# Kernel optimization log

Measured on AMD Instinct MI355X. Metric: run time of the kernel, lower is better.

## Reference

```python
import jax, jax.numpy as jnp
import numpy as np

D_MODEL = 1024
H = 16
D_K = D_MODEL // H  # 64


def setup_inputs() -> dict:
    key = jax.random.key(0)
    ks = jax.random.split(key, 10)
    s = 1.0 / np.sqrt(D_MODEL)
    x = jax.random.normal(ks[0], (4, 2048, D_MODEL), dtype=jnp.float32)
    # Per-head linear weights stacked: [H, d_model, d_k]
    Wq = jax.random.uniform(ks[1], (H, D_MODEL, D_K), jnp.float32, -s, s)
    bq = jax.random.uniform(ks[2], (H, D_K), jnp.float32, -s, s)
    Wk = jax.random.uniform(ks[3], (H, D_MODEL, D_K), jnp.float32, -s, s)
    bk = jax.random.uniform(ks[4], (H, D_K), jnp.float32, -s, s)
    Wv = jax.random.uniform(ks[5], (H, D_MODEL, D_K), jnp.float32, -s, s)
    bv = jax.random.uniform(ks[6], (H, D_K), jnp.float32, -s, s)
    so = 1.0 / np.sqrt(H * D_K)
    Wo = jax.random.uniform(ks[7], (H * D_K, D_MODEL), jnp.float32, -so, so)
    bo = jax.random.uniform(ks[8], (D_MODEL,), jnp.float32, -so, so)
    return {"x": x, "Wq": Wq, "bq": bq, "Wk": Wk, "bk": bk, "Wv": Wv, "bv": bv, "Wo": Wo, "bo": bo}


def reference(x, Wq, bq, Wk, bk, Wv, bv, Wo, bo):
    # x: [B, S, D]; Wq/Wk/Wv: [H, D, d_k]; b*: [H, d_k]
    q = jnp.einsum('bsd,hdk->bhsk', x, Wq) + bq[None, :, None, :]
    k = jnp.einsum('bsd,hdk->bhsk', x, Wk) + bk[None, :, None, :]
    v = jnp.einsum('bsd,hdk->bhsk', x, Wv) + bv[None, :, None, :]
    scores = jnp.einsum('bhqk,bhsk->bhqs', q, k) / np.sqrt(D_K)
    S = x.shape[1]
    causal = jnp.triu(jnp.ones((S, S), dtype=bool), k=1)  # True above diagonal
    scores = jnp.where(causal, -jnp.inf, scores)
    attn = jax.nn.softmax(scores, axis=-1)
    ctx = jnp.einsum('bhqs,bhsk->bhqk', attn, v)  # [B, H, S, d_k]
    B = x.shape[0]
    # concat heads: torch cats head outputs along last dim -> [B, S, H*d_k]
    ctx = jnp.transpose(ctx, (0, 2, 1, 3)).reshape(B, S, H * D_K)
    return ctx @ Wo + bo
```

## Files before the change

kernel.cpp:

```cpp
#include <hip/hip_runtime.h>
#include <hip/hip_bf16.h>

typedef unsigned short u16;
typedef __attribute__((ext_vector_type(8))) short short8;
typedef __attribute__((ext_vector_type(4))) short short4v;
typedef __attribute__((ext_vector_type(4))) float floatx4;

#define D_MODEL 1024
#define NH 16
#define SEQ 2048
#define BATCH 4
#define M_ROWS 8192
#define N_QKV 3072
#define PS_LD 72

__device__ __forceinline__ u16 f2u(float f) {
    __hip_bfloat16 h = __float2bfloat16(f);
    u16 u; __builtin_memcpy(&u, &h, 2); return u;
}

__device__ __forceinline__ void async_copy16(const u16* g, u16* l) {
    __builtin_amdgcn_global_load_lds(
        (const __attribute__((address_space(1))) unsigned int*)(g),
        (__attribute__((address_space(3))) unsigned int*)(l),
        16, 0, 0);
}

__global__ __launch_bounds__(256) void prep(
    const float* __restrict__ x,
    const float* __restrict__ Wq, const float* __restrict__ Wk,
    const float* __restrict__ Wv, const float* __restrict__ Wo,
    const float* __restrict__ bq, const float* __restrict__ bk,
    const float* __restrict__ bv, const float* __restrict__ bo,
    u16* __restrict__ xb, u16* __restrict__ Wpt, u16* __restrict__ Wot,
    float* __restrict__ biasp)
{
    __shared__ u16 T[64 * 72];
    const int tid = threadIdx.x;
    const int blk = blockIdx.x;

    if (blk < 4096) {
        size_t i = ((size_t)blk * 256 + tid) * 8;
        float4 f0 = *(const float4*)&x[i];
        float4 f1 = *(const float4*)&x[i + 4];
        u16 t[8] = {f2u(f0.x), f2u(f0.y), f2u(f0.z), f2u(f0.w),
                    f2u(f1.x), f2u(f1.y), f2u(f1.z), f2u(f1.w)};
        *(short8*)&xb[i] = *(short8*)t;
        return;
    }
    if (blk == 5120) {
        #pragma unroll
        for (int j = 0; j < 16; j++) {
            int idx = j * 256 + tid;
            float v;
            if (idx < 1024)      v = bq[idx] * 0.125f;
            else if (idx < 2048) v = bk[idx - 1024];
            else if (idx < 3072) v = bv[idx - 2048];
            else                 v = bo[idx - 3072];
            biasp[idx] = v;
        }
        return;
    }
    const int wb = blk - 4096;
    const int r = tid >> 2, s4 = (tid & 3) * 16;
    if (wb < 768) {
        int sel = wb / 256, rem = wb % 256;
        int h = rem >> 4, ktile = rem & 15;
        const float* W = (sel == 0) ? Wq : ((sel == 1) ? Wk : Wv);
        const float scale = (sel == 0) ? 0.125f : 1.0f;
        const float* src = W + ((size_t)h * 1024 + ktile * 64 + r) * 64 + s4;
        #pragma unroll
        for (int i = 0; i < 16; i++) T[(s4 + i) * 72 + r] = f2u(src[i] * scale);
        __syncthreads();
        u16 tmp[16];
        #pragma unroll
        for (int i = 0; i < 16; i++) tmp[i] = T[r * 72 + s4 + i];
        u16* dst = Wpt + ((size_t)sel * 1024 + h * 64 + r) * 1024 + ktile * 64 + s4;
        *(short8*)&dst[0] = *(short8*)&tmp[0];
        *(short8*)&dst[8] = *(short8*)&tmp[8];
    } else {
        int rem = wb - 768;
        int nt = rem >> 4, kt2 = rem & 15;
        const float* src = Wo + ((size_t)kt2 * 64 + r) * 1024 + nt * 64 + s4;
        #pragma unroll
        for (int i = 0; i < 16; i++) T[(s4 + i) * 72 + r] = f2u(src[i]);
        __syncthreads();
        u16 tmp[16];
        #pragma unroll
        for (int i = 0; i < 16; i++) tmp[i] = T[r * 72 + s4 + i];
        u16* dst = Wot + ((size_t)nt * 64 + r) * 1024 + kt2 * 64 + s4;
        *(short8*)&dst[0] = *(short8*)&tmp[0];
        *(short8*)&dst[8] = *(short8*)&tmp[8];
    }
}

__global__ __launch_bounds__(256) void vtrans(const u16* __restrict__ QKV,
                                              u16* __restrict__ Vtg) {
    __shared__ u16 T[64 * 72];
    const int bh = blockIdx.x, kt = blockIdx.y;
    const int b = bh >> 4, h = bh & 15;
    const int tid = threadIdx.x;
    const int r = tid >> 2, s4 = (tid & 3) * 16;
    const u16* vp = QKV + (size_t)(b * SEQ + kt * 64 + r) * N_QKV + 2 * D_MODEL + h * 64 + s4;
    *(short8*)&T[r * 72 + s4]     = *(const short8*)&vp[0];
    *(short8*)&T[r * 72 + s4 + 8] = *(const short8*)&vp[8];
    __syncthreads();
    u16 tmp[16];
    #pragma unroll
    for (int i = 0; i < 16; i++) tmp[i] = T[(s4 + i) * 72 + r];
    u16* op = Vtg + ((size_t)bh * 64 + r) * SEQ + kt * 64 + s4;
    *(short8*)&op[0] = *(short8*)&tmp[0];
    *(short8*)&op[8] = *(short8*)&tmp[8];
}

template <typename OT>
__global__ __launch_bounds__(256) void gemm128(
    const u16* __restrict__ A, const u16* __restrict__ Bt,
    const float* __restrict__ bias, OT* __restrict__ C,
    int M, int N, int K)
{
    __shared__ u16 As[128 * 64];
    __shared__ u16 Bs[128 * 64];
    const int tid = threadIdx.x;
    const int w = tid >> 6, lane = tid & 63;
    const int l16 = lane & 15, quad = lane >> 4;
    const int bn = blockIdx.x * 128, bm = blockIdx.y * 128;
    const int wr = (w >> 1) * 64, wc = (w & 1) * 64;

    floatx4 acc[4][4];
    #pragma unroll
    for (int i = 0; i < 4; i++)
        #pragma unroll
        for (int j = 0; j < 4; j++) acc[i][j] = (floatx4){0.f, 0.f, 0.f, 0.f};

    for (int k0 = 0; k0 < K; k0 += 64) {
        #pragma unroll
        for (int c = 0; c < 4; c++) {
            const int off = (w * 4 + c) * 1024 + lane * 16;
            const int row = off >> 7, seg = (off >> 4) & 7;
            async_copy16(A  + (size_t)(bm + row) * K + k0 + seg * 8, &As[(w * 4 + c) * 512]);
            async_copy16(Bt + (size_t)(bn + row) * K + k0 + seg * 8, &Bs[(w * 4 + c) * 512]);
        }
        __syncthreads();
        #pragma unroll
        for (int kc = 0; kc < 2; kc++) {
            short8 a[4], b[4];
            #pragma unroll
            for (int i = 0; i < 4; i++)
                a[i] = *(short8*)&As[(wr + i * 16 + l16) * 64 + kc * 32 + quad * 8];
            #pragma unroll
            for (int i = 0; i < 4; i++)
                b[i] = *(short8*)&Bs[(wc + i * 16 + l16) * 64 + kc * 32 + quad * 8];
            #pragma unroll
            for (int mm = 0; mm < 4; mm++)
                #pragma unroll
                for (int nn = 0; nn < 4; nn++)
                    acc[mm][nn] = __builtin_amdgcn_mfma_f32_16x16x32_bf16(
                        a[mm], b[nn], acc[mm][nn], 0, 0, 0);
        }
        __syncthreads();
    }

    #pragma unroll
    for (int nn = 0; nn < 4; nn++) {
        const int col = bn + wc + nn * 16 + l16;
        const float bi = bias[col];
        #pragma unroll
        for (int mm = 0; mm < 4; mm++) {
            const int row = bm + wr + mm * 16 + quad * 4;
            #pragma unroll
            for (int r = 0; r < 4; r++) {
                float v = acc[mm][nn][r] + bi;
                if constexpr (sizeof(OT) == 2) ((u16*)C)[(size_t)(row + r) * N + col] = f2u(v);
                else                           C[(size_t)(row + r) * N + col] = v;
            }
        }
    }
}

__global__ __launch_bounds__(256) void attn_mfma(
    const u16* __restrict__ QKV, const u16* __restrict__ Vtg, u16* __restrict__ ctx)
{
    __shared__ u16 Ks[2][64 * 64];
    __shared__ u16 Vs[2][64 * 64];
    __shared__ u16 Ps[128 * PS_LD];

    const int bh = blockIdx.x;
    const int qt = (int)(gridDim.y - 1) - (int)blockIdx.y;
    const int b = bh >> 4, h = bh & 15;
    const int tid = threadIdx.x;
    const int w = tid >> 6, lane = tid & 63;
    const int l16 = lane & 15, quad = lane >> 4;

    const int r0 = tid >> 3,        c0 = tid & 7;
    const int r1 = (256 + tid) >> 3, c1 = tid & 7;
    const int sw0 = c0 ^ (r0 & 7), sw1 = c1 ^ (r1 & 7);

    short8 q[2][2];
    #pragma unroll
    for (int m = 0; m < 2; m++) {
        const u16* qp = QKV + (size_t)(b * SEQ + qt * 128 + w * 32 + m * 16 + l16) * N_QKV + h * 64;
        q[m][0] = *(const short8*)&qp[quad * 8];
        q[m][1] = *(const short8*)&qp[32 + quad * 8];
    }

    floatx4 O[2][4];
    #pragma unroll
    for (int m = 0; m < 2; m++)
        #pragma unroll
        for (int i = 0; i < 4; i++) O[m][i] = (floatx4){0.f, 0.f, 0.f, 0.f};
    float li[2] = {0.f, 0.f};

    const int nkt = 2 * qt + 2;
    const int qrow_w_max = qt * 128 + w * 32 + 31;

    const size_t kbase = (size_t)(b * SEQ) * N_QKV + D_MODEL + h * 64;
    const size_t vbase = (size_t)bh * 64 * SEQ;

    {
        float4 ka = *(const float4*)(QKV + kbase + (size_t)(0 + r0) * N_QKV + c0 * 8);
        float4 kb = *(const float4*)(QKV + kbase + (size_t)(0 + r1) * N_QKV + c1 * 8);
        float4 va = *(const float4*)(Vtg + vbase + (size_t)r0 * SEQ + 0 + c0 * 8);
        float4 vb = *(const float4*)(Vtg + vbase + (size_t)r1 * SEQ + 0 + c1 * 8);
        *(float4*)&Ks[0][r0 * 64 + sw0 * 8] = ka;
        *(float4*)&Ks[0][r1 * 64 + sw1 * 8] = kb;
        *(float4*)&Vs[0][r0 * 64 + sw0 * 8] = va;
        *(float4*)&Vs[0][r1 * 64 + sw1 * 8] = vb;
    }
    __syncthreads();

    for (int kt = 0; kt < nkt; kt++) {
        const int buf = kt & 1;
        const bool pre = (kt + 1 < nkt);
        float4 ka, kb, va, vb;
        if (pre) {
            const int t1 = (kt + 1) * 64;
            ka = *(const float4*)(QKV + kbase + (size_t)(t1 + r0) * N_QKV + c0 * 8);
            kb = *(const float4*)(QKV + kbase + (size_t)(t1 + r1) * N_QKV + c1 * 8);
            va = *(const float4*)(Vtg + vbase + (size_t)r0 * SEQ + t1 + c0 * 8);
            vb = *(const float4*)(Vtg + vbase + (size_t)r1 * SEQ + t1 + c1 * 8);
        }

        if (kt * 64 <= qrow_w_max) {
            short8 kf[4][2];
            #pragma unroll
            for (int ns = 0; ns < 4; ns++) {
                const int rr = ns * 16 + l16, rs = rr & 7;
                kf[ns][0] = *(short8*)&Ks[buf][rr * 64 + (quad ^ rs) * 8];
                kf[ns][1] = *(short8*)&Ks[buf][rr * 64 + ((4 + quad) ^ rs) * 8];
            }
            const bool needMask = (kt * 64 + 63 > qt * 128 + w * 32);

            #pragma unroll
            for (int m = 0; m < 2; m++) {
                floatx4 z[4];
                #pragma unroll
                for (int ns = 0; ns < 4; ns++) {
                    floatx4 t = (floatx4){0.f, 0.f, 0.f, 0.f};
                    t = __builtin_amdgcn_mfma_f32_16x16x32_bf16(kf[ns][0], q[m][0], t, 0, 0, 0);
                    t = __builtin_amdgcn_mfma_f32_16x16x32_bf16(kf[ns][1], q[m][1], t, 0, 0, 0);
                    z[ns] = t;
                }
                const int qrow_g = qt * 128 + w * 32 + m * 16 + l16;
                const int prow = (w * 32 + m * 16 + l16) * PS_LD;
                float sum = 0.f;
                #pragma unroll
                for (int ns = 0; ns < 4; ns++) {
                    u16 pk[4];
                    #pragma unroll
                    for (int r = 0; r < 4; r++) {
                        float s = z[ns][r];
                        const int key = kt * 64 + ns * 16 + quad * 4 + r;
                        if (needMask && key > qrow_g) s = -INFINITY;
                        float p = __expf(s - 8.0f);
                        pk[r] = f2u(p);
                        sum += p;
                    }
                    *(short4v*)&Ps[prow + ns * 16 + quad * 4] = *(short4v*)pk;
                }
                sum += __shfl_xor(sum, 16);
                sum += __shfl_xor(sum, 32);
                li[m] += sum;
            }

            short8 vf[4][2];
            #pragma unroll
            for (int ds = 0; ds < 4; ds++) {
                const int rr = ds * 16 + l16, rs = rr & 7;
                vf[ds][0] = *(short8*)&Vs[buf][rr * 64 + (quad ^ rs) * 8];
                vf[ds][1] = *(short8*)&Vs[buf][rr * 64 + ((4 + quad) ^ rs) * 8];
            }
            #pragma unroll
            for (int m = 0; m < 2; m++) {
                const int prow = (w * 32 + m * 16 + l16) * PS_LD;
                short8 p0 = *(short8*)&Ps[prow + quad * 8];
                short8 p1 = *(short8*)&Ps[prow + 32 + quad * 8];
                #pragma unroll
                for (int ds = 0; ds < 4; ds++) {
                    O[m][ds] = __builtin_amdgcn_mfma_f32_16x16x32_bf16(vf[ds][0], p0, O[m][ds], 0, 0, 0);
                    O[m][ds] = __builtin_amdgcn_mfma_f32_16x16x32_bf16(vf[ds][1], p1, O[m][ds], 0, 0, 0);
                }
            }
        }

        if (pre) {
            const int nb = buf ^ 1;
            *(float4*)&Ks[nb][r0 * 64 + sw0 * 8] = ka;
            *(float4*)&Ks[nb][r1 * 64 + sw1 * 8] = kb;
            *(float4*)&Vs[nb][r0 * 64 + sw0 * 8] = va;
            *(float4*)&Vs[nb][r1 * 64 + sw1 * 8] = vb;
        }
        __syncthreads();
    }

    #pragma unroll
    for (int m = 0; m < 2; m++) {
        const float inv = 1.0f / li[m];
        const size_t base = (size_t)(b * SEQ + qt * 128 + w * 32 + m * 16 + l16) * D_MODEL + h * 64;
        #pragma unroll
        for (int ds = 0; ds < 4; ds++) {
            u16 o[4];
            #pragma unroll
            for (int r = 0; r < 4; r++) o[r] = f2u(O[m][ds][r] * inv);
            *(short4v*)&ctx[base + ds * 16 + quad * 4] = *(short4v*)o;
        }
    }
}

extern "C" void kernel_launch(void* const* d_in, const int* in_sizes, int n_in,
                              void* d_out, int out_size, void* d_ws, size_t ws_size,
                              hipStream_t stream) {
    const float* x  = (const float*)d_in[0];
    const float* Wq = (const float*)d_in[1];
    const float* bq = (const float*)d_in[2];
    const float* Wk = (const float*)d_in[3];
    const float* bk = (const float*)d_in[4];
    const float* Wv = (const float*)d_in[5];
    const float* bv = (const float*)d_in[6];
    const float* Wo = (const float*)d_in[7];
    const float* bo = (const float*)d_in[8];
    float* out = (float*)d_out;

    char* ws = (char*)d_ws;
    float* biasp = (float*)ws;
    u16*   Wpt   = (u16*)(ws + 0x10000);
    u16*   Wot   = (u16*)(ws + 0x620000);
    u16*   xb    = (u16*)(ws + 0x840000);
    u16*   Vtg   = xb;
    u16*   QKV   = (u16*)(ws + 0x1840000);
    u16*   ctx   = (u16*)(ws + 0x4840000);

    prep<<<5121, 256, 0, stream>>>(x, Wq, Wk, Wv, Wo, bq, bk, bv, bo,
                                   xb, Wpt, Wot, biasp);

    gemm128<u16><<<dim3(N_QKV / 128, M_ROWS / 128), 256, 0, stream>>>(
        xb, Wpt, biasp, QKV, M_ROWS, N_QKV, D_MODEL);

    vtrans<<<dim3(64, 32), 256, 0, stream>>>(QKV, Vtg);

    attn_mfma<<<dim3(BATCH * NH, SEQ / 128), 256, 0, stream>>>(QKV, Vtg, ctx);

    gemm128<float><<<dim3(D_MODEL / 128, M_ROWS / 128), 256, 0, stream>>>(
        ctx, Wot, biasp + N_QKV, out, M_ROWS, D_MODEL, D_MODEL);
}
```

Measured before the change: 294.5 us.

## Fuse x fp32-to-bf16 conversion into QKV GEMM and register-prefetch with swizzled LDS

Drops the separate x-to-bf16 conversion pass. The QKV GEMM now reads fp32 x directly and converts it while storing to LDS. Both GEMMs replace the direct global-to-LDS async copies with register prefetch of the next K tile, overlapped with the MFMA work on the current tile, and use XOR-swizzled LDS layouts to avoid bank conflicts. The fp32 A operand is twice as wide, so the QKV GEMM now reads twice the bytes for x, 24 times over (once per N tile), and needs more registers and an extra barrier per iteration.

```diff
diff --git a/kernel.cpp b/kernel.cpp
--- a/kernel.cpp
+++ b/kernel.cpp
@@ -19,36 +19,18 @@
     u16 u; __builtin_memcpy(&u, &h, 2); return u;
 }
 
-__device__ __forceinline__ void async_copy16(const u16* g, u16* l) {
-    __builtin_amdgcn_global_load_lds(
-        (const __attribute__((address_space(1))) unsigned int*)(g),
-        (__attribute__((address_space(3))) unsigned int*)(l),
-        16, 0, 0);
-}
-
 __global__ __launch_bounds__(256) void prep(
-    const float* __restrict__ x,
     const float* __restrict__ Wq, const float* __restrict__ Wk,
     const float* __restrict__ Wv, const float* __restrict__ Wo,
     const float* __restrict__ bq, const float* __restrict__ bk,
     const float* __restrict__ bv, const float* __restrict__ bo,
-    u16* __restrict__ xb, u16* __restrict__ Wpt, u16* __restrict__ Wot,
-    float* __restrict__ biasp)
+    u16* __restrict__ Wpt, u16* __restrict__ Wot, float* __restrict__ biasp)
 {
     __shared__ u16 T[64 * 72];
     const int tid = threadIdx.x;
     const int blk = blockIdx.x;
 
-    if (blk < 4096) {
-        size_t i = ((size_t)blk * 256 + tid) * 8;
-        float4 f0 = *(const float4*)&x[i];
-        float4 f1 = *(const float4*)&x[i + 4];
-        u16 t[8] = {f2u(f0.x), f2u(f0.y), f2u(f0.z), f2u(f0.w),
-                    f2u(f1.x), f2u(f1.y), f2u(f1.z), f2u(f1.w)};
-        *(short8*)&xb[i] = *(short8*)t;
-        return;
-    }
-    if (blk == 5120) {
+    if (blk == 1024) {
         #pragma unroll
         for (int j = 0; j < 16; j++) {
             int idx = j * 256 + tid;
@@ -61,10 +43,9 @@
         }
         return;
     }
-    const int wb = blk - 4096;
     const int r = tid >> 2, s4 = (tid & 3) * 16;
-    if (wb < 768) {
-        int sel = wb / 256, rem = wb % 256;
+    if (blk < 768) {
+        int sel = blk / 256, rem = blk % 256;
         int h = rem >> 4, ktile = rem & 15;
         const float* W = (sel == 0) ? Wq : ((sel == 1) ? Wk : Wv);
         const float scale = (sel == 0) ? 0.125f : 1.0f;
@@ -79,7 +60,7 @@
         *(short8*)&dst[0] = *(short8*)&tmp[0];
         *(short8*)&dst[8] = *(short8*)&tmp[8];
     } else {
-        int rem = wb - 768;
+        int rem = blk - 768;
         int nt = rem >> 4, kt2 = rem & 15;
         const float* src = Wo + ((size_t)kt2 * 64 + r) * 1024 + nt * 64 + s4;
         #pragma unroll
@@ -113,9 +94,9 @@
     *(short8*)&op[8] = *(short8*)&tmp[8];
 }
 
-template <typename OT>
+template <typename AT, typename OT>
 __global__ __launch_bounds__(256) void gemm128(
-    const u16* __restrict__ A, const u16* __restrict__ Bt,
+    const AT* __restrict__ A, const u16* __restrict__ Bt,
     const float* __restrict__ bias, OT* __restrict__ C,
     int M, int N, int K)
 {
@@ -127,30 +108,74 @@
     const int bn = blockIdx.x * 128, bm = blockIdx.y * 128;
     const int wr = (w >> 1) * 64, wc = (w & 1) * 64;
 
+    const int rj = tid >> 3, c = tid & 7;
+
     floatx4 acc[4][4];
     #pragma unroll
     for (int i = 0; i < 4; i++)
         #pragma unroll
         for (int j = 0; j < 4; j++) acc[i][j] = (floatx4){0.f, 0.f, 0.f, 0.f};
 
+    constexpr int AW = (sizeof(AT) == 4) ? 2 : 1;
+    float4 areg[4][AW];
+    float4 breg[4];
+
+    #pragma unroll
+    for (int i = 0; i < 4; i++) {
+        const int row = rj + i * 32;
+        const AT* ap = A + (size_t)(bm + row) * K + c * 8;
+        if constexpr (AW == 2) {
+            areg[i][0] = *(const float4*)((const float*)ap);
+            areg[i][1] = *(const float4*)((const float*)ap + 4);
+        } else {
+            areg[i][0] = *(const float4*)ap;
+        }
+        breg[i] = *(const float4*)(Bt + (size_t)(bn + row) * K + c * 8);
+    }
+    #pragma unroll
+    for (int i = 0; i < 4; i++) {
+        const int row = rj + i * 32;
+        const int slot = (c ^ (row & 7)) * 8;
+        if constexpr (AW == 2) {
+            const float* f0 = (const float*)&areg[i][0];
+            const float* f1 = (const float*)&areg[i][1];
+            u16 t[8] = {f2u(f0[0]), f2u(f0[1]), f2u(f0[2]), f2u(f0[3]),
+                        f2u(f1[0]), f2u(f1[1]), f2u(f1[2]), f2u(f1[3])};
+            *(float4*)&As[row * 64 + slot] = *(float4*)t;
+        } else {
+            *(float4*)&As[row * 64 + slot] = areg[i][0];
+        }
+        *(float4*)&Bs[row * 64 + slot] = breg[i];
+    }
+    __syncthreads();
+
     for (int k0 = 0; k0 < K; k0 += 64) {
-        #pragma unroll
-        for (int c = 0; c < 4; c++) {
-            const int off = (w * 4 + c) * 1024 + lane * 16;
-            const int row = off >> 7, seg = (off >> 4) & 7;
-            async_copy16(A  + (size_t)(bm + row) * K + k0 + seg * 8, &As[(w * 4 + c) * 512]);
-            async_copy16(Bt + (size_t)(bn + row) * K + k0 + seg * 8, &Bs[(w * 4 + c) * 512]);
-        }
-        __syncthreads();
+        const bool pre = (k0 + 64 < K);
+        if (pre) {
+            #pragma unroll
+            for (int i = 0; i < 4; i++) {
+                const int row = rj + i * 32;
+                const AT* ap = A + (size_t)(bm + row) * K + k0 + 64 + c * 8;
+                if constexpr (AW == 2) {
+                    areg[i][0] = *(const float4*)((const float*)ap);
+                    areg[i][1] = *(const float4*)((const float*)ap + 4);
+                } else {
+                    areg[i][0] = *(const float4*)ap;
+                }
+                breg[i] = *(const float4*)(Bt + (size_t)(bn + row) * K + k0 + 64 + c * 8);
+            }
+        }
+
         #pragma unroll
         for (int kc = 0; kc < 2; kc++) {
             short8 a[4], b[4];
             #pragma unroll
-            for (int i = 0; i < 4; i++)
-                a[i] = *(short8*)&As[(wr + i * 16 + l16) * 64 + kc * 32 + quad * 8];
-            #pragma unroll
-            for (int i = 0; i < 4; i++)
-                b[i] = *(short8*)&Bs[(wc + i * 16 + l16) * 64 + kc * 32 + quad * 8];
+            for (int i = 0; i < 4; i++) {
+                const int ra = wr + i * 16 + l16;
+                a[i] = *(short8*)&As[ra * 64 + ((kc * 4 + quad) ^ (ra & 7)) * 8];
+                const int rb = wc + i * 16 + l16;
+                b[i] = *(short8*)&Bs[rb * 64 + ((kc * 4 + quad) ^ (rb & 7)) * 8];
+            }
             #pragma unroll
             for (int mm = 0; mm < 4; mm++)
                 #pragma unroll
@@ -158,7 +183,26 @@
                     acc[mm][nn] = __builtin_amdgcn_mfma_f32_16x16x32_bf16(
                         a[mm], b[nn], acc[mm][nn], 0, 0, 0);
         }
-        __syncthreads();
+
+        if (pre) {
+            __syncthreads();
+            #pragma unroll
+            for (int i = 0; i < 4; i++) {
+                const int row = rj + i * 32;
+                const int slot = (c ^ (row & 7)) * 8;
+                if constexpr (AW == 2) {
+                    const float* f0 = (const float*)&areg[i][0];
+                    const float* f1 = (const float*)&areg[i][1];
+                    u16 t[8] = {f2u(f0[0]), f2u(f0[1]), f2u(f0[2]), f2u(f0[3]),
+                                f2u(f1[0]), f2u(f1[1]), f2u(f1[2]), f2u(f1[3])};
+                    *(float4*)&As[row * 64 + slot] = *(float4*)t;
+                } else {
+                    *(float4*)&As[row * 64 + slot] = areg[i][0];
+                }
+                *(float4*)&Bs[row * 64 + slot] = breg[i];
+            }
+            __syncthreads();
+        }
     }
 
     #pragma unroll
@@ -192,7 +236,7 @@
     const int w = tid >> 6, lane = tid & 63;
     const int l16 = lane & 15, quad = lane >> 4;
 
-    const int r0 = tid >> 3,        c0 = tid & 7;
+    const int r0 = tid >> 3,         c0 = tid & 7;
     const int r1 = (256 + tid) >> 3, c1 = tid & 7;
     const int sw0 = c0 ^ (r0 & 7), sw1 = c1 ^ (r1 & 7);
 
@@ -218,10 +262,10 @@
     const size_t vbase = (size_t)bh * 64 * SEQ;
 
     {
-        float4 ka = *(const float4*)(QKV + kbase + (size_t)(0 + r0) * N_QKV + c0 * 8);
-        float4 kb = *(const float4*)(QKV + kbase + (size_t)(0 + r1) * N_QKV + c1 * 8);
-        float4 va = *(const float4*)(Vtg + vbase + (size_t)r0 * SEQ + 0 + c0 * 8);
-        float4 vb = *(const float4*)(Vtg + vbase + (size_t)r1 * SEQ + 0 + c1 * 8);
+        float4 ka = *(const float4*)(QKV + kbase + (size_t)r0 * N_QKV + c0 * 8);
+        float4 kb = *(const float4*)(QKV + kbase + (size_t)r1 * N_QKV + c1 * 8);
+        float4 va = *(const float4*)(Vtg + vbase + (size_t)r0 * SEQ + c0 * 8);
+        float4 vb = *(const float4*)(Vtg + vbase + (size_t)r1 * SEQ + c1 * 8);
         *(float4*)&Ks[0][r0 * 64 + sw0 * 8] = ka;
         *(float4*)&Ks[0][r1 * 64 + sw1 * 8] = kb;
         *(float4*)&Vs[0][r0 * 64 + sw0 * 8] = va;
@@ -345,21 +389,20 @@
     float* biasp = (float*)ws;
     u16*   Wpt   = (u16*)(ws + 0x10000);
     u16*   Wot   = (u16*)(ws + 0x620000);
-    u16*   xb    = (u16*)(ws + 0x840000);
-    u16*   Vtg   = xb;
-    u16*   QKV   = (u16*)(ws + 0x1840000);
+    u16*   QKV   = (u16*)(ws + 0x840000);
+    u16*   Vtg   = (u16*)(ws + 0x3840000);
     u16*   ctx   = (u16*)(ws + 0x4840000);
 
-    prep<<<5121, 256, 0, stream>>>(x, Wq, Wk, Wv, Wo, bq, bk, bv, bo,
-                                   xb, Wpt, Wot, biasp);
-
-    gemm128<u16><<<dim3(N_QKV / 128, M_ROWS / 128), 256, 0, stream>>>(
-        xb, Wpt, biasp, QKV, M_ROWS, N_QKV, D_MODEL);
+    prep<<<1025, 256, 0, stream>>>(Wq, Wk, Wv, Wo, bq, bk, bv, bo,
+                                   Wpt, Wot, biasp);
+
+    gemm128<float, u16><<<dim3(N_QKV / 128, M_ROWS / 128), 256, 0, stream>>>(
+        x, Wpt, biasp, QKV, M_ROWS, N_QKV, D_MODEL);
 
     vtrans<<<dim3(64, 32), 256, 0, stream>>>(QKV, Vtg);
 
     attn_mfma<<<dim3(BATCH * NH, SEQ / 128), 256, 0, stream>>>(QKV, Vtg, ctx);
 
-    gemm128<float><<<dim3(D_MODEL / 128, M_ROWS / 128), 256, 0, stream>>>(
+    gemm128<u16, float><<<dim3(D_MODEL / 128, M_ROWS / 128), 256, 0, stream>>>(
         ctx, Wot, biasp + N_QKV, out, M_ROWS, D_MODEL, D_MODEL);
 }
```

Result: slower. 470.2 us (+59.7%).
